# Optimization experiments

Hardware: AMD Instinct MI355X
Metric: run time of the kernel (lower is better)

## Reference

```python
import jax, jax.numpy as jnp
import numpy as np

N_NODES = 100_000
N_EDGES = 1_600_000
N_GRAPHS = 1_000
NODES_PER_GRAPH = 100
N_NODE_FEATS = 64
DIM_STATE = 32
DIM_OUT = 64
DIM_NODE_EMB = 64
HID = 128
HEADS = 8
BASES = 4


def _lin(key, out_f, in_f, bias=True):
    k1, k2 = jax.random.split(key)
    lim = 1.0 / np.sqrt(in_f)
    w = jax.random.uniform(k1, (out_f, in_f), minval=-lim, maxval=lim, dtype=jnp.float32)
    if not bias:
        return w
    b = jax.random.uniform(k2, (out_f,), minval=-lim, maxval=lim, dtype=jnp.float32)
    return w, b


def setup_inputs() -> dict:
    key = jax.random.key(0)
    ks = jax.random.split(key, 16)
    x = jax.random.normal(ks[0], (N_NODES, N_NODE_FEATS), dtype=jnp.float32)
    edge_index = jax.random.randint(ks[1], (2, N_EDGES), 0, N_NODES, dtype=jnp.int32)
    batch = jnp.arange(N_NODES, dtype=jnp.int32) // NODES_PER_GRAPH  # sorted segment ids
    n_atoms = jnp.full((N_GRAPHS, 1), NODES_PER_GRAPH, dtype=jnp.int32)  # consistent with batch
    z_e = jax.random.normal(ks[2], (N_GRAPHS, DIM_STATE), dtype=jnp.float32)
    nfc_w, nfc_b = _lin(ks[3], HID, N_NODE_FEATS)
    # EGConv: bases Linear(in, (out//heads)*bases, no bias); comb Linear(in, heads*bases); bias (out,)
    gc1_bases_w = _lin(ks[4], (HID // HEADS) * BASES, HID, bias=False)
    gc1_comb_w, gc1_comb_b = _lin(ks[5], HEADS * BASES, HID)
    gc1_bias = jnp.zeros((HID,), jnp.float32)
    gc2_bases_w = _lin(ks[6], (DIM_NODE_EMB // HEADS) * BASES, HID, bias=False)
    gc2_comb_w, gc2_comb_b = _lin(ks[7], HEADS * BASES, HID)
    gc2_bias = jnp.zeros((DIM_NODE_EMB,), jnp.float32)
    attn_w, attn_b = _lin(ks[8], 1, DIM_NODE_EMB + DIM_STATE)
    fcg_w, fcg_b = _lin(ks[9], DIM_OUT, DIM_NODE_EMB)
    fccg_w, fccg_b = _lin(ks[10], DIM_OUT, DIM_NODE_EMB)
    return {"x": x, "edge_index": edge_index, "batch": batch, "n_atoms": n_atoms, "z_e": z_e,
            "nfc_w": nfc_w, "nfc_b": nfc_b,
            "gc1_bases_w": gc1_bases_w, "gc1_comb_w": gc1_comb_w, "gc1_comb_b": gc1_comb_b, "gc1_bias": gc1_bias,
            "gc2_bases_w": gc2_bases_w, "gc2_comb_w": gc2_comb_w, "gc2_comb_b": gc2_comb_b, "gc2_bias": gc2_bias,
            "attn_w": attn_w, "attn_b": attn_b, "fcg_w": fcg_w, "fcg_b": fcg_b, "fccg_w": fccg_w, "fccg_b": fccg_b}


def _egconv(h, src, dst, bases_w, comb_w, comb_b, bias, heads=HEADS, nbases=BASES):
    # PyG EGConv with aggregators=['symnorm'], add_self_loops=True
    n = h.shape[0]
    out_ch = bias.shape[0]
    deg = jnp.ones((n,), h.dtype).at[dst].add(1.0)          # in-degree + self loop
    dis = jax.lax.rsqrt(deg)                                 # deg^-1/2
    b = h @ bases_w.T                                        # [n, nbases*(out_ch//heads)]
    # symnorm aggregation incl. self-loop term dis_i^2 * b_i
    agg = ((dis * dis)[:, None] * b).at[dst].add((dis[src] * dis[dst])[:, None] * b[src])
    w = (h @ comb_w.T + comb_b).reshape(n, heads, nbases)    # [n, H, B]
    agg = agg.reshape(n, nbases, out_ch // heads)            # [n, B, F/H]
    return jnp.einsum('nhb,nbf->nhf', w, agg).reshape(n, out_ch) + bias


def reference(x, edge_index, batch, n_atoms, z_e, nfc_w, nfc_b,
              gc1_bases_w, gc1_comb_w, gc1_comb_b, gc1_bias,
              gc2_bases_w, gc2_comb_w, gc2_comb_b, gc2_bias,
              attn_w, attn_b, fcg_w, fcg_b, fccg_w, fccg_b):
    src, dst = edge_index[0], edge_index[1]
    h = jax.nn.elu(x @ nfc_w.T + nfc_b)
    h = jax.nn.elu(_egconv(h, src, dst, gc1_bases_w, gc1_comb_w, gc1_comb_b, gc1_bias))
    h = jax.nn.elu(_egconv(h, src, dst, gc2_bases_w, gc2_comb_w, gc2_comb_b, gc2_bias))
    h = h / jnp.maximum(jnp.linalg.norm(h, axis=1, keepdims=True), 1e-12)  # L2 normalize
    z_a = jax.ops.segment_sum(h, batch, num_segments=N_GRAPHS) @ fcg_w.T + fcg_b
    z_rep = jnp.repeat(z_e, n_atoms[:, 0], axis=0, total_repeat_length=N_NODES)
    logits = jnp.concatenate([h, z_rep], axis=1) @ attn_w.T + attn_b + 1e-16  # [N,1]
    m = jax.ops.segment_max(logits, batch, num_segments=N_GRAPHS)
    e = jnp.exp(logits - m[batch])
    denom = jax.ops.segment_sum(e, batch, num_segments=N_GRAPHS) + 1e-16
    attns = e / denom[batch]
    z_c = jax.ops.segment_sum(attns * h, batch, num_segments=N_GRAPHS) @ fccg_w.T + fccg_b
    return z_a, z_c, h
```

## Files before the change

### kernel.cpp

```cpp
#include <hip/hip_runtime.h>
#include <hip/hip_bf16.h>
#include <math.h>

#define N_NODES  100000
#define N_EDGES  1600000
#define N_GRAPHS 1000
#define NPG      100
#define NBKT     391
#define BCAP     5120
#define EPB      4096
#define NBE      ((N_EDGES + EPB - 1) / EPB)
#define GBA      ((N_NODES + 63) / 64)

typedef float  f32x4 __attribute__((ext_vector_type(4)));
typedef short  s16x8 __attribute__((ext_vector_type(8)));

__device__ __forceinline__ float elu_f(float x) {
    return x > 0.0f ? x : expm1f(x);
}
__device__ __forceinline__ float bf2f(unsigned int u16) {
    union { unsigned int i; float f; } v; v.i = u16 << 16; return v.f;
}
__device__ __forceinline__ unsigned short f2bf(float f) {
    __hip_bfloat16 h = __float2bfloat16(f);
    return *reinterpret_cast<unsigned short*>(&h);
}
__device__ __forceinline__ s16x8 cvt8(const float4& a, const float4& b) {
    s16x8 o;
    o[0]=(short)f2bf(a.x); o[1]=(short)f2bf(a.y); o[2]=(short)f2bf(a.z); o[3]=(short)f2bf(a.w);
    o[4]=(short)f2bf(b.x); o[5]=(short)f2bf(b.y); o[6]=(short)f2bf(b.z); o[7]=(short)f2bf(b.w);
    return o;
}

__global__ __launch_bounds__(512) void setup_k(
    int* __restrict__ bkt_cur,
    const float* __restrict__ w0, const float* __restrict__ w1c, const float* __restrict__ w1w,
    const float* __restrict__ w2c, const float* __restrict__ w2w, unsigned short* __restrict__ wb)
{
    int t = threadIdx.x;
    if (blockIdx.x == 0 && t < NBKT) bkt_cur[t] = t * BCAP;
    int i = blockIdx.x * 512 + t;
    float v;
    if (i < 8192)       v = w0[i];
    else if (i < 16384) v = w1c[i - 8192];
    else if (i < 20480) v = w1w[i - 16384];
    else if (i < 24576) v = w2c[i - 20480];
    else if (i < 28672) v = w2w[i - 24576];
    else return;
    wb[i] = f2bf(v);
}

__global__ __launch_bounds__(256) void scatterA_k(
    const float* __restrict__ x, const unsigned short* __restrict__ wb,
    const float* __restrict__ b0, const float* __restrict__ bw,
    unsigned short* __restrict__ c1out, float* __restrict__ w1out, int M,
    const int* __restrict__ ei, int* __restrict__ bkt_cur, unsigned int* __restrict__ pairs)
{
    __shared__ union {
        struct { int h[NBKT]; int base[NBKT]; } sc;
        unsigned short hT[64][136];
    } u;

    const int t = threadIdx.x;

    if (blockIdx.x >= GBA) {
        const int eb = blockIdx.x - GBA;
        int* h = u.sc.h;
        int* base = u.sc.base;
        for (int i = t; i < NBKT; i += 256) h[i] = 0;
        __syncthreads();
        const int4* src4 = (const int4*)ei;
        const int4* dst4 = (const int4*)(ei + N_EDGES);
        int i0 = eb * (EPB / 4);
        for (int i = t; i < EPB / 4; i += 256) {
            int g = i0 + i;
            if (g < N_EDGES / 4) {
                int4 d = dst4[g];
                atomicAdd(&h[d.x >> 8], 1);
                atomicAdd(&h[d.y >> 8], 1);
                atomicAdd(&h[d.z >> 8], 1);
                atomicAdd(&h[d.w >> 8], 1);
            }
        }
        __syncthreads();
        for (int i = t; i < NBKT; i += 256) {
            int c = h[i];
            base[i] = c ? atomicAdd(&bkt_cur[i], c) : 0;
            h[i] = 0;
        }
        __syncthreads();
        for (int i = t; i < EPB / 4; i += 256) {
            int g = i0 + i;
            if (g < N_EDGES / 4) {
                int4 s4 = src4[g];
                int4 d4 = dst4[g];
                int b, r;
                b = d4.x >> 8; r = atomicAdd(&h[b], 1); pairs[base[b] + r] = ((unsigned)s4.x << 8) | (d4.x & 255);
                b = d4.y >> 8; r = atomicAdd(&h[b], 1); pairs[base[b] + r] = ((unsigned)s4.y << 8) | (d4.y & 255);
                b = d4.z >> 8; r = atomicAdd(&h[b], 1); pairs[base[b] + r] = ((unsigned)s4.z << 8) | (d4.z & 255);
                b = d4.w >> 8; r = atomicAdd(&h[b], 1); pairs[base[b] + r] = ((unsigned)s4.w << 8) | (d4.w & 255);
            }
        }
        return;
    }

    const unsigned short* W0b = wb;
    const unsigned short* Wcb = wb + 8192;
    const unsigned short* Wwb = wb + 16384;

    const int wave = t >> 6, lane = t & 63;
    const int lr = lane & 15, lk = lane >> 4;
    const int blockRow = blockIdx.x * 64;

    {
        const int wr = wave >> 1, wc = wave & 1;
        f32x4 acc[2][4];
        #pragma unroll
        for (int rt = 0; rt < 2; ++rt)
            #pragma unroll
            for (int ct = 0; ct < 4; ++ct) acc[rt][ct] = (f32x4){0.f,0.f,0.f,0.f};

        #pragma unroll
        for (int kt = 0; kt < 2; ++kt) {
            const int k0 = kt * 32 + lk * 8;
            s16x8 afr[2];
            #pragma unroll
            for (int rt = 0; rt < 2; ++rt) {
                int r = blockRow + (wr * 2 + rt) * 16 + lr;
                r = (r < M) ? r : (M - 1);
                const float* ap = x + (size_t)r * 64 + k0;
                afr[rt] = cvt8(*(const float4*)ap, *(const float4*)(ap + 4));
            }
            s16x8 bfr[4];
            #pragma unroll
            for (int ct = 0; ct < 4; ++ct) {
                int n = (wc * 4 + ct) * 16 + lr;
                bfr[ct] = *(const s16x8*)(W0b + (size_t)n * 64 + k0);
            }
            #pragma unroll
            for (int rt = 0; rt < 2; ++rt)
                #pragma unroll
                for (int ct = 0; ct < 4; ++ct)
                    acc[rt][ct] = __builtin_amdgcn_mfma_f32_16x16x32_bf16(afr[rt], bfr[ct], acc[rt][ct], 0, 0, 0);
        }
        #pragma unroll
        for (int rt = 0; rt < 2; ++rt) {
            int lmb = (wr * 2 + rt) * 16 + lk * 4;
            #pragma unroll
            for (int j = 0; j < 4; ++j) {
                #pragma unroll
                for (int ct = 0; ct < 4; ++ct) {
                    int n = (wc * 4 + ct) * 16 + lr;
                    u.hT[lmb + j][n] = f2bf(elu_f(acc[rt][ct][j] + b0[n]));
                }
            }
        }
    }
    __syncthreads();

    {
        f32x4 acc[6];
        #pragma unroll
        for (int ct = 0; ct < 6; ++ct) acc[ct] = (f32x4){0.f,0.f,0.f,0.f};
        #pragma unroll
        for (int kt = 0; kt < 4; ++kt) {
            const int k0 = kt * 32 + lk * 8;
            s16x8 af = *(const s16x8*)&u.hT[wave * 16 + lr][k0];
            #pragma unroll
            for (int ct = 0; ct < 6; ++ct) {
                int n = ct * 16 + lr;
                const unsigned short* wp = (n < 64) ? (Wcb + (size_t)n * 128 + k0)
                                                    : (Wwb + (size_t)(n - 64) * 128 + k0);
                acc[ct] = __builtin_amdgcn_mfma_f32_16x16x32_bf16(af, *(const s16x8*)wp, acc[ct], 0, 0, 0);
            }
        }
        int mbase = blockRow + wave * 16 + lk * 4;
        #pragma unroll
        for (int j = 0; j < 4; ++j) {
            int m = mbase + j;
            if (m >= M) continue;
            #pragma unroll
            for (int ct = 0; ct < 6; ++ct) {
                int n = ct * 16 + lr;
                float v = acc[ct][j];
                if (n < 64) c1out[(size_t)m * 64 + n] = f2bf(v);
                else        w1out[(size_t)m * 32 + (n - 64)] = v + bw[n - 64];
            }
        }
    }
}

__global__ __launch_bounds__(256) void bucket_csr_k(const unsigned int* __restrict__ pairs,
                                                    const int* __restrict__ bkt_cur,
                                                    int* __restrict__ starts,
                                                    int* __restrict__ cnt,
                                                    float* __restrict__ dis,
                                                    int* __restrict__ srclist)
{
    __shared__ int s[256];
    __shared__ int cur[256];
    const int b = blockIdx.x, t = threadIdx.x;
    const int lo = b * BCAP;
    const int hi = bkt_cur[b];
    const int n0 = b << 8;
    const int nn = min(256, N_NODES - n0);

    s[t] = 0;
    __syncthreads();
    for (int i = lo + t; i < hi; i += 256) {
        unsigned int p = pairs[i];
        atomicAdd(&s[p & 255], 1);
    }
    __syncthreads();
    int v = s[t];
    __syncthreads();
    s[t] = v;
    __syncthreads();
    #pragma unroll
    for (int off = 1; off < 256; off <<= 1) {
        int u = (t >= off) ? s[t - off] : 0;
        __syncthreads();
        s[t] += u;
        __syncthreads();
    }
    int ex = lo + s[t] - v;
    if (t < nn) {
        starts[n0 + t] = ex;
        cnt[n0 + t] = v;
        dis[n0 + t] = rsqrtf(1.0f + (float)v);
    }
    cur[t] = ex;
    __syncthreads();
    for (int i = lo + t; i < hi; i += 256) {
        unsigned int p = pairs[i];
        int pos = atomicAdd(&cur[p & 255], 1);
        srclist[pos] = (int)(p >> 8);
    }
}

__global__ __launch_bounds__(256) void mgemmL2_k(
    const unsigned short* __restrict__ Ab, const unsigned short* __restrict__ wb,
    const float* __restrict__ bw, const float* __restrict__ dis,
    unsigned short* __restrict__ c2out, float* __restrict__ w2out, int M)
{
    const unsigned short* Wcb = wb + 20480;
    const unsigned short* Wwb = wb + 24576;

    const int t = threadIdx.x;
    const int wave = t >> 6, lane = t & 63;
    const int wr = wave >> 1, wc = wave & 1;
    const int lr = lane & 15, lk = lane >> 4;
    const int blockRow = blockIdx.x * 64;

    f32x4 acc[2][2];
    #pragma unroll
    for (int rt = 0; rt < 2; ++rt)
        #pragma unroll
        for (int ct = 0; ct < 2; ++ct) acc[rt][ct] = (f32x4){0.f,0.f,0.f,0.f};

    #pragma unroll
    for (int kt = 0; kt < 4; ++kt) {
        const int k0 = kt * 32 + lk * 8;
        s16x8 afr[2];
        #pragma unroll
        for (int rt = 0; rt < 2; ++rt) {
            int r = blockRow + (wr * 2 + rt) * 16 + lr;
            r = (r < M) ? r : (M - 1);
            afr[rt] = *(const s16x8*)(Ab + (size_t)r * 128 + k0);
        }
        s16x8 bfr[2];
        #pragma unroll
        for (int ct = 0; ct < 2; ++ct) {
            int n = (wc * 2 + ct) * 16 + lr;
            const unsigned short* wp = (n < 32) ? (Wcb + (size_t)n * 128 + k0)
                                                : (Wwb + (size_t)(n - 32) * 128 + k0);
            bfr[ct] = *(const s16x8*)wp;
        }
        #pragma unroll
        for (int rt = 0; rt < 2; ++rt)
            #pragma unroll
            for (int ct = 0; ct < 2; ++ct)
                acc[rt][ct] = __builtin_amdgcn_mfma_f32_16x16x32_bf16(afr[rt], bfr[ct], acc[rt][ct], 0, 0, 0);
    }

    #pragma unroll
    for (int rt = 0; rt < 2; ++rt) {
        int mbase = blockRow + (wr * 2 + rt) * 16 + lk * 4;
        #pragma unroll
        for (int j = 0; j < 4; ++j) {
            int m = mbase + j;
            if (m >= M) continue;
            float dsc = dis[m];
            #pragma unroll
            for (int ct = 0; ct < 2; ++ct) {
                int n = (wc * 2 + ct) * 16 + lr;
                float v = acc[rt][ct][j];
                if (n < 32) c2out[(size_t)m * 32 + n] = f2bf(dsc * v);
                else        w2out[(size_t)m * 32 + (n - 32)] = v + bw[n - 32];
            }
        }
    }
}

__global__ __launch_bounds__(256) void gather1_k(
    const int* __restrict__ starts, const int* __restrict__ cnt,
    const int* __restrict__ srclist, const unsigned short* __restrict__ c,
    const float* __restrict__ w1, const float* __restrict__ dis,
    const float* __restrict__ bias, unsigned short* __restrict__ h2b)
{
    __shared__ float aggS[4][68];

    const int t = threadIdx.x;
    const int nn   = t >> 6;
    const int lane = t & 63;
    const int q    = lane & 15;
    const int slot = lane >> 4;
    const int n    = blockIdx.x * 4 + nn;

    const int s0 = starts[n];
    const int cn = cnt[n];
    float a0 = 0.f, a1 = 0.f, a2 = 0.f, a3 = 0.f;
    if (slot == 0) {
        float dsn = dis[n];
        uint2 u = *(const uint2*)(c + (size_t)n * 64 + q * 4);
        a0 = dsn * bf2f(u.x & 0xffff); a1 = dsn * bf2f(u.x >> 16);
        a2 = dsn * bf2f(u.y & 0xffff); a3 = dsn * bf2f(u.y >> 16);
    }
    for (int j = slot; j < cn; j += 4) {
        int src = srclist[s0 + j];
        float ds = dis[src];
        uint2 u = *(const uint2*)(c + (size_t)src * 64 + q * 4);
        a0 = fmaf(ds, bf2f(u.x & 0xffff), a0); a1 = fmaf(ds, bf2f(u.x >> 16), a1);
        a2 = fmaf(ds, bf2f(u.y & 0xffff), a2); a3 = fmaf(ds, bf2f(u.y >> 16), a3);
    }
    a0 += __shfl_xor(a0, 16, 64); a0 += __shfl_xor(a0, 32, 64);
    a1 += __shfl_xor(a1, 16, 64); a1 += __shfl_xor(a1, 32, 64);
    a2 += __shfl_xor(a2, 16, 64); a2 += __shfl_xor(a2, 32, 64);
    a3 += __shfl_xor(a3, 16, 64); a3 += __shfl_xor(a3, 32, 64);
    if (slot == 0) {
        aggS[nn][q * 4 + 0] = a0;
        aggS[nn][q * 4 + 1] = a1;
        aggS[nn][q * 4 + 2] = a2;
        aggS[nn][q * 4 + 3] = a3;
    }
    __syncthreads();

    const float dn = dis[n];
    const float* wr = w1 + (size_t)n * 32;
    unsigned short* out = h2b + (size_t)n * 128;
    #pragma unroll
    for (int r = 0; r < 2; ++r) {
        int j = r * 64 + lane;
        int hh = j >> 4, f = j & 15;
        float4 wv = *(const float4*)(wr + hh * 4);
        float s = wv.x * aggS[nn][0 * 16 + f] + wv.y * aggS[nn][1 * 16 + f]
                + wv.z * aggS[nn][2 * 16 + f] + wv.w * aggS[nn][3 * 16 + f];
        out[j] = f2bf(elu_f(s * dn + bias[j]));
    }
}

__global__ __launch_bounds__(256) void gather2_k(
    const int* __restrict__ starts, const int* __restrict__ cnt,
    const int* __restrict__ srclist, const unsigned short* __restrict__ c,
    const float* __restrict__ w2, const float* __restrict__ dis,
    const float* __restrict__ bias, float* __restrict__ hout)
{
    __shared__ float aggS[4][36];

    const int t = threadIdx.x;
    const int nn   = t >> 6;
    const int lane = t & 63;
    const int q    = lane & 15;
    const int slot = lane >> 4;
    const int n    = blockIdx.x * 4 + nn;

    const int s0 = starts[n];
    const int cn = cnt[n];
    float a0 = 0.f, a1 = 0.f;
    if (slot == 0) {
        unsigned int u = *(const unsigned int*)(c + (size_t)n * 32 + q * 2);
        a0 = bf2f(u & 0xffff); a1 = bf2f(u >> 16);
    }
    for (int j = slot; j < cn; j += 4) {
        int src = srclist[s0 + j];
        unsigned int u = *(const unsigned int*)(c + (size_t)src * 32 + q * 2);
        a0 += bf2f(u & 0xffff); a1 += bf2f(u >> 16);
    }
    a0 += __shfl_xor(a0, 16, 64); a0 += __shfl_xor(a0, 32, 64);
    a1 += __shfl_xor(a1, 16, 64); a1 += __shfl_xor(a1, 32, 64);
    if (slot == 0) {
        aggS[nn][q * 2 + 0] = a0;
        aggS[nn][q * 2 + 1] = a1;
    }
    __syncthreads();

    const float dn = dis[n];
    const int hh = lane >> 3, f = lane & 7;
    float4 wv = *(const float4*)(w2 + (size_t)n * 32 + hh * 4);
    float s = wv.x * aggS[nn][0 * 8 + f] + wv.y * aggS[nn][1 * 8 + f]
            + wv.z * aggS[nn][2 * 8 + f] + wv.w * aggS[nn][3 * 8 + f];
    float sv = elu_f(s * dn + bias[lane]);

    float tot = sv * sv;
    #pragma unroll
    for (int o = 1; o < 64; o <<= 1) tot += __shfl_xor(tot, o, 64);
    float inv = 1.0f / fmaxf(sqrtf(tot), 1e-12f);
    hout[(size_t)n * 64 + lane] = sv * inv;
}

__global__ __launch_bounds__(128) void graph_k(const float* __restrict__ h,
                                               const float* __restrict__ z_e,
                                               const float* __restrict__ aw,
                                               const float* __restrict__ ab,
                                               const float* __restrict__ fcgw,
                                               const float* __restrict__ fcgb,
                                               const float* __restrict__ fccgw,
                                               const float* __restrict__ fccgb,
                                               float* __restrict__ z_a,
                                               float* __restrict__ z_c)
{
    __shared__ float Hs[NPG * 64];
    __shared__ float sumh[64], wsh[64], lg[NPG], ex[NPG];
    __shared__ float red[2];
    int g = blockIdx.x, t = threadIdx.x;
    const float* hg = h + (size_t)g * NPG * 64;
    for (int idx = t; idx < NPG * 64; idx += 128) Hs[idx] = hg[idx];
    __syncthreads();

    if (t < 64) {
        float s = 0.0f;
        for (int n = 0; n < NPG; ++n) s += Hs[n * 64 + t];
        sumh[t] = s;
    }
    __syncthreads();

    if (t < 64) {
        float acc = fcgb[t];
        for (int f = 0; f < 64; ++f) acc = fmaf(sumh[f], fcgw[t * 64 + f], acc);
        z_a[(size_t)g * 64 + t] = acc;
    }
    if (t < NPG) {
        float zd = 0.0f;
        for (int q = 0; q < 32; ++q) zd = fmaf(z_e[(size_t)g * 32 + q], aw[64 + q], zd);
        float dot = 0.0f;
        for (int k0 = 0; k0 < 64; ++k0) {
            int k = (k0 + t) & 63;
            dot = fmaf(Hs[t * 64 + k], aw[k], dot);
        }
        lg[t] = dot + zd + ab[0] + 1e-16f;
    }
    __syncthreads();

    if (t < 64) {
        float m = -INFINITY;
        for (int n = t; n < NPG; n += 64) m = fmaxf(m, lg[n]);
        #pragma unroll
        for (int o = 1; o < 64; o <<= 1) m = fmaxf(m, __shfl_xor(m, o, 64));
        if (t == 0) red[0] = m;
    }
    __syncthreads();
    float m = red[0];
    if (t < NPG) ex[t] = expf(lg[t] - m);
    __syncthreads();
    if (t < 64) {
        float s = 0.0f;
        for (int n = t; n < NPG; n += 64) s += ex[n];
        #pragma unroll
        for (int o = 1; o < 64; o <<= 1) s += __shfl_xor(s, o, 64);
        if (t == 0) red[1] = s + 1e-16f;
    }
    __syncthreads();
    float inv_denom = 1.0f / red[1];
    if (t < 64) {
        float a = 0.0f;
        for (int n = 0; n < NPG; ++n) a = fmaf(ex[n], Hs[n * 64 + t], a);
        wsh[t] = a * inv_denom;
    }
    __syncthreads();
    if (t < 64) {
        float acc = fccgb[t];
        for (int f = 0; f < 64; ++f) acc = fmaf(wsh[f], fccgw[t * 64 + f], acc);
        z_c[(size_t)g * 64 + t] = acc;
    }
}

extern "C" void kernel_launch(void* const* d_in, const int* in_sizes, int n_in,
                              void* d_out, int out_size, void* d_ws, size_t ws_size,
                              hipStream_t stream)
{
    const float* x     = (const float*)d_in[0];
    const int*   ei    = (const int*)d_in[1];
    const float* z_e   = (const float*)d_in[4];
    const float* nfc_w = (const float*)d_in[5];
    const float* nfc_b = (const float*)d_in[6];
    const float* g1bw  = (const float*)d_in[7];
    const float* g1cw  = (const float*)d_in[8];
    const float* g1cb  = (const float*)d_in[9];
    const float* g1b   = (const float*)d_in[10];
    const float* g2bw  = (const float*)d_in[11];
    const float* g2cw  = (const float*)d_in[12];
    const float* g2cb  = (const float*)d_in[13];
    const float* g2b   = (const float*)d_in[14];
    const float* aw    = (const float*)d_in[15];
    const float* ab    = (const float*)d_in[16];
    const float* fcgw  = (const float*)d_in[17];
    const float* fcgb  = (const float*)d_in[18];
    const float* fccgw = (const float*)d_in[19];
    const float* fccgb = (const float*)d_in[20];

    float* ws        = (float*)d_ws;
    float* dis       = ws;
    int*   cnt       = (int*)(ws + 102400);
    int*   starts    = cnt + 102400;
    int*   bkt_cur   = starts + 102400;
    int*   srclist   = bkt_cur + 512;
    float* hbuf      = (float*)(srclist + 2002048);
    float* c1f       = hbuf + 6400000;
    float* w1        = c1f + 3200000;
    float* c2f       = w1 + 3200000;
    float* w2        = c2f + 1600000;
    unsigned short* wb = (unsigned short*)(w2 + 3200000);
    unsigned int*  pairs = (unsigned int*)hbuf;
    unsigned short* hb = (unsigned short*)hbuf;
    unsigned short* c1 = (unsigned short*)c1f;
    unsigned short* c2 = (unsigned short*)c2f;

    float* z_a  = (float*)d_out;
    float* z_c  = z_a + (size_t)N_GRAPHS * 64;
    float* hout = z_a + (size_t)2 * N_GRAPHS * 64;

    setup_k<<<57, 512, 0, stream>>>(bkt_cur, nfc_w, g1bw, g1cw, g2bw, g2cw, wb);
    scatterA_k<<<GBA + NBE, 256, 0, stream>>>(x, wb, nfc_b, g1cb, c1, w1, N_NODES,
                                              ei, bkt_cur, pairs);
    bucket_csr_k<<<NBKT, 256, 0, stream>>>(pairs, bkt_cur, starts, cnt, dis, srclist);
    gather1_k<<<N_NODES / 4, 256, 0, stream>>>(starts, cnt, srclist, c1, w1, dis, g1b, hb);
    mgemmL2_k<<<GBA, 256, 0, stream>>>(hb, wb, g2cb, dis, c2, w2, N_NODES);
    gather2_k<<<N_NODES / 4, 256, 0, stream>>>(starts, cnt, srclist, c2, w2, dis, g2b, hout);
    graph_k<<<N_GRAPHS, 128, 0, stream>>>(hout, z_e, aw, ab, fcgw, fcgb, fccgw, fccgb, z_a, z_c);
}
```

Measured before the change: 239.9 us.

## Fuse layer-2 gather with per-graph readout and enlarge edge bucketing blocks

The second-layer neighbor gather, ELU and L2 normalization now run inside the per-graph readout kernel. Each block handles one graph, and its four waves loop over that graph's 100 nodes. The normalized rows go straight into shared memory, so the readout no longer re-reads h from global memory, and one launch is removed. Separately, each edge-bucketing block now handles four times as many edges, and those blocks are moved ahead of the GEMM blocks in the grid. In exchange, far fewer blocks are in flight for the latency-bound gather, so each wave processes its nodes serially with less parallelism to hide latency.

```diff
diff --git a/kernel.cpp b/kernel.cpp
--- a/kernel.cpp
+++ b/kernel.cpp
@@ -8,7 +8,7 @@
 #define NPG      100
 #define NBKT     391
 #define BCAP     5120
-#define EPB      4096
+#define EPB      16384
 #define NBE      ((N_EDGES + EPB - 1) / EPB)
 #define GBA      ((N_NODES + 63) / 64)
 
@@ -63,8 +63,8 @@
 
     const int t = threadIdx.x;
 
-    if (blockIdx.x >= GBA) {
-        const int eb = blockIdx.x - GBA;
+    if (blockIdx.x < NBE) {
+        const int eb = blockIdx.x;
         int* h = u.sc.h;
         int* base = u.sc.base;
         for (int i = t; i < NBKT; i += 256) h[i] = 0;
@@ -110,7 +110,7 @@
 
     const int wave = t >> 6, lane = t & 63;
     const int lr = lane & 15, lk = lane >> 4;
-    const int blockRow = blockIdx.x * 64;
+    const int blockRow = (blockIdx.x - NBE) * 64;
 
     {
         const int wr = wave >> 1, wc = wave & 1;
@@ -359,72 +359,62 @@
     }
 }
 
-__global__ __launch_bounds__(256) void gather2_k(
+__global__ __launch_bounds__(256) void graphfused_k(
     const int* __restrict__ starts, const int* __restrict__ cnt,
     const int* __restrict__ srclist, const unsigned short* __restrict__ c,
     const float* __restrict__ w2, const float* __restrict__ dis,
-    const float* __restrict__ bias, float* __restrict__ hout)
-{
+    const float* __restrict__ bias,
+    const float* __restrict__ z_e, const float* __restrict__ aw, const float* __restrict__ ab,
+    const float* __restrict__ fcgw, const float* __restrict__ fcgb,
+    const float* __restrict__ fccgw, const float* __restrict__ fccgb,
+    float* __restrict__ hout, float* __restrict__ z_a, float* __restrict__ z_c)
+{
+    __shared__ float Hs[NPG * 64];
     __shared__ float aggS[4][36];
-
-    const int t = threadIdx.x;
-    const int nn   = t >> 6;
-    const int lane = t & 63;
+    __shared__ float sumh[64], wsh[64], lg[NPG], ex[NPG];
+    __shared__ float red[2];
+
+    const int g = blockIdx.x, t = threadIdx.x;
+    const int wave = t >> 6, lane = t & 63;
     const int q    = lane & 15;
     const int slot = lane >> 4;
-    const int n    = blockIdx.x * 4 + nn;
-
-    const int s0 = starts[n];
-    const int cn = cnt[n];
-    float a0 = 0.f, a1 = 0.f;
-    if (slot == 0) {
-        unsigned int u = *(const unsigned int*)(c + (size_t)n * 32 + q * 2);
-        a0 = bf2f(u & 0xffff); a1 = bf2f(u >> 16);
-    }
-    for (int j = slot; j < cn; j += 4) {
-        int src = srclist[s0 + j];
-        unsigned int u = *(const unsigned int*)(c + (size_t)src * 32 + q * 2);
-        a0 += bf2f(u & 0xffff); a1 += bf2f(u >> 16);
-    }
-    a0 += __shfl_xor(a0, 16, 64); a0 += __shfl_xor(a0, 32, 64);
-    a1 += __shfl_xor(a1, 16, 64); a1 += __shfl_xor(a1, 32, 64);
-    if (slot == 0) {
-        aggS[nn][q * 2 + 0] = a0;
-        aggS[nn][q * 2 + 1] = a1;
-    }
-    __syncthreads();
-
-    const float dn = dis[n];
-    const int hh = lane >> 3, f = lane & 7;
-    float4 wv = *(const float4*)(w2 + (size_t)n * 32 + hh * 4);
-    float s = wv.x * aggS[nn][0 * 8 + f] + wv.y * aggS[nn][1 * 8 + f]
-            + wv.z * aggS[nn][2 * 8 + f] + wv.w * aggS[nn][3 * 8 + f];
-    float sv = elu_f(s * dn + bias[lane]);
-
-    float tot = sv * sv;
-    #pragma unroll
-    for (int o = 1; o < 64; o <<= 1) tot += __shfl_xor(tot, o, 64);
-    float inv = 1.0f / fmaxf(sqrtf(tot), 1e-12f);
-    hout[(size_t)n * 64 + lane] = sv * inv;
-}
-
-__global__ __launch_bounds__(128) void graph_k(const float* __restrict__ h,
-                                               const float* __restrict__ z_e,
-                                               const float* __restrict__ aw,
-                                               const float* __restrict__ ab,
-                                               const float* __restrict__ fcgw,
-                                               const float* __restrict__ fcgb,
-                                               const float* __restrict__ fccgw,
-                                               const float* __restrict__ fccgb,
-                                               float* __restrict__ z_a,
-                                               float* __restrict__ z_c)
-{
-    __shared__ float Hs[NPG * 64];
-    __shared__ float sumh[64], wsh[64], lg[NPG], ex[NPG];
-    __shared__ float red[2];
-    int g = blockIdx.x, t = threadIdx.x;
-    const float* hg = h + (size_t)g * NPG * 64;
-    for (int idx = t; idx < NPG * 64; idx += 128) Hs[idx] = hg[idx];
+
+    for (int it = 0; it < 25; ++it) {
+        const int ln = it * 4 + wave;
+        const int n  = g * NPG + ln;
+        const int s0 = starts[n];
+        const int cn = cnt[n];
+        float a0 = 0.f, a1 = 0.f;
+        if (slot == 0) {
+            unsigned int u = *(const unsigned int*)(c + (size_t)n * 32 + q * 2);
+            a0 = bf2f(u & 0xffff); a1 = bf2f(u >> 16);
+        }
+        for (int j = slot; j < cn; j += 4) {
+            int src = srclist[s0 + j];
+            unsigned int u = *(const unsigned int*)(c + (size_t)src * 32 + q * 2);
+            a0 += bf2f(u & 0xffff); a1 += bf2f(u >> 16);
+        }
+        a0 += __shfl_xor(a0, 16, 64); a0 += __shfl_xor(a0, 32, 64);
+        a1 += __shfl_xor(a1, 16, 64); a1 += __shfl_xor(a1, 32, 64);
+        if (slot == 0) {
+            aggS[wave][q * 2 + 0] = a0;
+            aggS[wave][q * 2 + 1] = a1;
+        }
+        const float dn = dis[n];
+        const int hh = lane >> 3, f = lane & 7;
+        float4 wv = *(const float4*)(w2 + (size_t)n * 32 + hh * 4);
+        float s = wv.x * aggS[wave][0 * 8 + f] + wv.y * aggS[wave][1 * 8 + f]
+                + wv.z * aggS[wave][2 * 8 + f] + wv.w * aggS[wave][3 * 8 + f];
+        float sv = elu_f(s * dn + bias[lane]);
+
+        float tot = sv * sv;
+        #pragma unroll
+        for (int o = 1; o < 64; o <<= 1) tot += __shfl_xor(tot, o, 64);
+        float inv = 1.0f / fmaxf(sqrtf(tot), 1e-12f);
+        float hv = sv * inv;
+        hout[(size_t)n * 64 + lane] = hv;
+        Hs[ln * 64 + lane] = hv;
+    }
     __syncthreads();
 
     if (t < 64) {
@@ -441,7 +431,7 @@
     }
     if (t < NPG) {
         float zd = 0.0f;
-        for (int q = 0; q < 32; ++q) zd = fmaf(z_e[(size_t)g * 32 + q], aw[64 + q], zd);
+        for (int qq = 0; qq < 32; ++qq) zd = fmaf(z_e[(size_t)g * 32 + qq], aw[64 + qq], zd);
         float dot = 0.0f;
         for (int k0 = 0; k0 < 64; ++k0) {
             int k = (k0 + t) & 63;
@@ -530,11 +520,12 @@
     float* hout = z_a + (size_t)2 * N_GRAPHS * 64;
 
     setup_k<<<57, 512, 0, stream>>>(bkt_cur, nfc_w, g1bw, g1cw, g2bw, g2cw, wb);
-    scatterA_k<<<GBA + NBE, 256, 0, stream>>>(x, wb, nfc_b, g1cb, c1, w1, N_NODES,
+    scatterA_k<<<NBE + GBA, 256, 0, stream>>>(x, wb, nfc_b, g1cb, c1, w1, N_NODES,
                                               ei, bkt_cur, pairs);
     bucket_csr_k<<<NBKT, 256, 0, stream>>>(pairs, bkt_cur, starts, cnt, dis, srclist);
     gather1_k<<<N_NODES / 4, 256, 0, stream>>>(starts, cnt, srclist, c1, w1, dis, g1b, hb);
     mgemmL2_k<<<GBA, 256, 0, stream>>>(hb, wb, g2cb, dis, c2, w2, N_NODES);
-    gather2_k<<<N_NODES / 4, 256, 0, stream>>>(starts, cnt, srclist, c2, w2, dis, g2b, hout);
-    graph_k<<<N_GRAPHS, 128, 0, stream>>>(hout, z_e, aw, ab, fcgw, fcgb, fccgw, fccgb, z_a, z_c);
-}
+    graphfused_k<<<N_GRAPHS, 256, 0, stream>>>(starts, cnt, srclist, c2, w2, dis, g2b,
+                                               z_e, aw, ab, fcgw, fcgb, fccgw, fccgb,
+                                               hout, z_a, z_c);
+}
```

After: 342.5 us. +42.8%, slower.
